# Kernel tuning notes

Measured on AMD Instinct MI355X. Metric: run time of the kernel, lower is better.

Reference implementation:

```python
import jax, jax.numpy as jnp
import numpy as np

MAX_JOINTS = 143

def setup_inputs() -> dict:
    key = jax.random.key(0)
    ks = jax.random.split(key, 8)
    d_model, latent_dim, feat = 256, 512, 13
    s = lambda n: 1.0 / np.sqrt(n)
    return {
        "z": jax.random.normal(ks[0], (32, latent_dim), jnp.float32),
        "W_latent": jax.random.normal(ks[1], (latent_dim, d_model), jnp.float32) * s(latent_dim),
        "b_latent": jnp.zeros((d_model,), jnp.float32),
        "joint_emb": jax.random.normal(ks[2], (MAX_JOINTS, d_model), jnp.float32),
        "frame_emb": jax.random.normal(ks[3], (120, d_model), jnp.float32),
        "ln_gamma": jnp.ones((d_model,), jnp.float32),
        "ln_beta": jnp.zeros((d_model,), jnp.float32),
        "W1": jax.random.normal(ks[4], (d_model, d_model), jnp.float32) * s(d_model),
        "b1": jnp.zeros((d_model,), jnp.float32),
        "W2": jax.random.normal(ks[5], (d_model, feat), jnp.float32) * s(d_model),
        "b2": jnp.zeros((feat,), jnp.float32),
        "max_frames": 120,
    }

def reference(z, W_latent, b_latent, joint_emb, frame_emb, ln_gamma, ln_beta, W1, b1, W2, b2, max_frames):
    # base: [B, d]
    base = z @ W_latent + b_latent
    fe = frame_emb[:max_frames]  # [F, d]
    # three-way broadcast sum -> [B, J, F, d]
    hidden = base[:, None, None, :] + joint_emb[None, :, None, :] + fe[None, None, :, :]
    # LayerNorm over last dim (eps=1e-5, torch default)
    mu = jnp.mean(hidden, axis=-1, keepdims=True)
    var = jnp.mean(jnp.square(hidden - mu), axis=-1, keepdims=True)
    h = (hidden - mu) * jax.lax.rsqrt(var + 1e-5) * ln_gamma + ln_beta
    # MLP: Linear -> exact GELU -> Linear
    h = jax.nn.gelu(h @ W1 + b1, approximate=False)
    out = h @ W2 + b2  # [B, J, F, feat]
    return jnp.transpose(out, (0, 1, 3, 2))  # [B, J, feat, F]
```

## Files before the change

kernel.cpp:

```cpp
#include <hip/hip_runtime.h>
#include <hip/hip_bf16.h>

typedef __bf16 bf16x8 __attribute__((ext_vector_type(8)));
typedef float  f32x4  __attribute__((ext_vector_type(4)));
typedef float  f32x2  __attribute__((ext_vector_type(2)));

#define B_  32
#define J_  143
#define F_  120
#define D_  256
#define L_  512
#define C_  13
#define M_  4576
#define NK  512
#define NNB 384
#define QB  9
#define GRIDC 509
#define CLS 260
#define PXS 388

static __device__ __forceinline__ unsigned short bits(__bf16 h) {
  return __builtin_bit_cast(unsigned short, h);
}

__device__ __forceinline__ f32x2 gelu2(f32x2 u) {
  f32x2 x2 = u * u;
  f32x2 t  = u * (x2 * -0.1029432f + -2.3022082f);
  f32x2 e;
  e.x = __builtin_amdgcn_exp2f(t.x);
  e.y = __builtin_amdgcn_exp2f(t.y);
  f32x2 d = e + 1.0f;
  f32x2 r;
  r.x = __builtin_amdgcn_rcpf(d.x);
  r.y = __builtin_amdgcn_rcpf(d.y);
  return u * r;
}

__global__ __launch_bounds__(256) void prep_kernel(
    const float* __restrict__ z, const float* __restrict__ Wl,
    const float* __restrict__ bl, const float* __restrict__ W1,
    const float* __restrict__ gamma, const float* __restrict__ beta,
    const float* __restrict__ b1, const float* __restrict__ fe,
    const float* __restrict__ W2,
    float* __restrict__ base, unsigned short* __restrict__ BT,
    float* __restrict__ bW1, float* __restrict__ Sfe, float* __restrict__ Sfe2,
    unsigned short* __restrict__ W2T, float* __restrict__ P2f) {
  const int t = threadIdx.x, bid = blockIdx.x;
  const int lane = t & 63, wv = t >> 6;
  __shared__ float zs[L_];
  __shared__ float ra[4], rb[4];
  __shared__ float fegl[256], gl2[256];

  if (bid < 32) {
    zs[t]       = z[bid * L_ + t];
    zs[t + 256] = z[bid * L_ + t + 256];
    __syncthreads();
    float acc = 0.f;
    #pragma unroll 32
    for (int k = 0; k < L_; ++k) acc = __builtin_fmaf(zs[k], Wl[k * D_ + t], acc);
    base[bid * D_ + t] = acc + bl[t];
    return;
  }
  if (bid < 432) {
    const int n = bid - 32;
    if (n < 256) {
      const float w1v = W1[t * D_ + n];
      float a = gamma[t] * w1v;
      float b = beta[t] * w1v;
      const float wg = a;
      #pragma unroll
      for (int m = 1; m < 64; m <<= 1) { a += __shfl_xor(a, m); b += __shfl_xor(b, m); }
      if (lane == 0) { ra[wv] = a; rb[wv] = b; }
      __syncthreads();
      const float cs = ra[0] + ra[1] + ra[2] + ra[3];
      if (t == 0) bW1[n] = rb[0] + rb[1] + rb[2] + rb[3] + b1[n];
      const float m = __builtin_fmaf(cs, -1.f / 256.f, wg);
      const __bf16 hi = (__bf16)m;
      const __bf16 lo = (__bf16)(m - (float)hi);
      BT[n * NK + t]       = bits(hi);
      BT[n * NK + 256 + t] = bits(lo);
    } else if (n < 376) {
      const int f = n - 256;
      const float v = fe[f * D_ + t];
      float a = v, b = v * v;
      #pragma unroll
      for (int m = 1; m < 64; m <<= 1) { a += __shfl_xor(a, m); b += __shfl_xor(b, m); }
      if (lane == 0) { ra[wv] = a; rb[wv] = b; }
      __syncthreads();
      if (t == 0) {
        Sfe[f]  = ra[0] + ra[1] + ra[2] + ra[3];
        Sfe2[f] = rb[0] + rb[1] + rb[2] + rb[3];
      }
      const __bf16 hi = (__bf16)v;
      const __bf16 lo = (__bf16)(v - (float)hi);
      BT[n * NK + t]       = bits(hi);
      BT[n * NK + 256 + t] = bits(lo);
    } else if (n < 384) {
      BT[n * NK + t] = 0; BT[n * NK + 256 + t] = 0;
    } else {
      const int c = n - 384;
      const float v = (c < C_) ? W2[t * C_ + c] : 0.f;
      W2T[c * D_ + t] = bits((__bf16)v);
    }
    return;
  }
  {
    const int f = bid - 432;
    const float fv = fe[f * D_ + t];
    const float gv = gamma[t];
    fegl[t] = fv * gv;
    gl2[t]  = gv;
    float a = fv;
    #pragma unroll
    for (int m = 1; m < 64; m <<= 1) a += __shfl_xor(a, m);
    if (lane == 0) ra[wv] = a;
    __syncthreads();
    const float sfe = ra[0] + ra[1] + ra[2] + ra[3];
    float acc1 = 0.f, acc2 = 0.f;
    #pragma unroll 8
    for (int k = 0; k < 256; ++k) {
      const float w = W1[k * D_ + t];
      acc1 = __builtin_fmaf(fegl[k], w, acc1);
      acc2 = __builtin_fmaf(gl2[k],  w, acc2);
    }
    P2f[f * D_ + t] = __builtin_fmaf(-sfe * (1.f / 256.f), acc2, acc1);
  }
}

__global__ __launch_bounds__(512, 4) void megaC_kernel(
    const float* __restrict__ base, const float* __restrict__ joint,
    const unsigned short* __restrict__ BT, const float* __restrict__ P2f,
    const float* __restrict__ bW1,
    const float* __restrict__ Sfe, const float* __restrict__ Sfe2,
    const unsigned short* __restrict__ W2T, const float* __restrict__ b2,
    float* __restrict__ out) {
  __shared__ float cl[16 * CLS];
  __shared__ float px[16 * PXS];
  __shared__ float bw[256];
  __shared__ float rstdl[QB][128];
  __shared__ float Scl[QB], Sc2l[QB];
  __shared__ __align__(16) unsigned short w2l[4096];

  const int tid  = threadIdx.x;
  const int lane = tid & 63, wv = tid >> 6;
  const int lrow = lane & 15, lgrp = lane >> 4;
  const int bj0  = blockIdx.x * QB;

  #pragma unroll
  for (int i = 0; i < 8; ++i) {
    const int idx = tid + i * 512;
    const int row = idx >> 8, col = idx & 255;
    float v = 0.f;
    if (row < QB) {
      const int bj = min(bj0 + row, M_ - 1);
      const int b = bj / J_, j = bj - b * J_;
      v = base[b * D_ + col] + joint[j * D_ + col];
    }
    cl[row * CLS + col] = v;
  }
  if (tid < 256) {
    bw[tid] = bW1[tid];
    const int rr = tid >> 4;
    const int b0 = tid * 32;
    const int sb = b0 ^ ((rr & 7) << 4);
    *(uint4*)((char*)w2l + sb)        = *(const uint4*)((const char*)W2T + b0);
    *(uint4*)((char*)w2l + (sb ^ 16)) = *(const uint4*)((const char*)W2T + b0 + 16);
  }
  __syncthreads();

  for (int r = wv; r < QB; r += 8) {
    const float4 v4 = *(const float4*)(cl + r * CLS + lane * 4);
    float s = v4.x + v4.y + v4.z + v4.w;
    float q = __builtin_fmaf(v4.x, v4.x,
              __builtin_fmaf(v4.y, v4.y,
              __builtin_fmaf(v4.z, v4.z, v4.w * v4.w)));
    #pragma unroll
    for (int m = 1; m < 64; m <<= 1) { s += __shfl_xor(s, m); q += __shfl_xor(q, m); }
    if (lane == 0) { Scl[r] = s; Sc2l[r] = q; }
  }

  {
    const int colbase = wv * 48;
    f32x4 acc[3] = {};
    #pragma unroll
    for (int s8 = 0; s8 < 8; ++s8) {
      const int k0 = s8 * 32 + lgrp * 8;
      const float4 c0 = *(const float4*)(cl + lrow * CLS + k0);
      const float4 c1 = *(const float4*)(cl + lrow * CLS + k0 + 4);
      const float cc[8] = {c0.x, c0.y, c0.z, c0.w, c1.x, c1.y, c1.z, c1.w};
      bf16x8 ahi, alo;
      #pragma unroll
      for (int e = 0; e < 8; ++e) {
        const __bf16 h = (__bf16)cc[e];
        ahi[e] = h;
        alo[e] = (__bf16)(cc[e] - (float)h);
      }
      bf16x8 bhi[3], blo[3];
      #pragma unroll
      for (int cf = 0; cf < 3; ++cf) {
        const unsigned short* bp =
            BT + (size_t)(colbase + cf * 16 + lrow) * NK + lgrp * 8;
        bhi[cf] = *(const bf16x8*)(bp + s8 * 32);
        blo[cf] = *(const bf16x8*)(bp + 256 + s8 * 32);
      }
      #pragma unroll
      for (int cf = 0; cf < 3; ++cf)
        acc[cf] = __builtin_amdgcn_mfma_f32_16x16x32_bf16(ahi, bhi[cf], acc[cf], 0, 0, 0);
      #pragma unroll
      for (int cf = 0; cf < 3; ++cf)
        acc[cf] = __builtin_amdgcn_mfma_f32_16x16x32_bf16(alo, bhi[cf], acc[cf], 0, 0, 0);
      #pragma unroll
      for (int cf = 0; cf < 3; ++cf)
        acc[cf] = __builtin_amdgcn_mfma_f32_16x16x32_bf16(ahi, blo[cf], acc[cf], 0, 0, 0);
    }
    #pragma unroll
    for (int cf = 0; cf < 3; ++cf)
      #pragma unroll
      for (int r4 = 0; r4 < 4; ++r4)
        px[(lgrp * 4 + r4) * PXS + colbase + cf * 16 + lrow] = acc[cf][r4];
  }
  __syncthreads();

  #pragma unroll
  for (int i = 0; i < 3; ++i) {
    const int idx = tid + i * 512;
    if (idx < QB * 128) {
      const int q = idx >> 7;
      const int fr = idx & 127;
      const int fc = fr < F_ ? fr : F_ - 1;
      const float X = px[q * PXS + 256 + fc];
      const float mu = (Scl[q] + Sfe[fc]) * (1.f / 256.f);
      const float ms = __builtin_fmaf(2.f, X, Sc2l[q] + Sfe2[fc]) * (1.f / 256.f);
      rstdl[q][fr] = rsqrtf(ms - mu * mu + 1e-5f);
    }
  }
  __syncthreads();

  const int r0 = wv * 16 + lrow;
  const int f0 = r0 < F_ ? r0 : F_ - 1;
  float rs[QB];
  #pragma unroll
  for (int q = 0; q < QB; ++q) rs[q] = rstdl[q][r0];
  const float* __restrict__ q0p = P2f + f0 * D_ + lgrp * 8;

  float4 qa0 = *(const float4*)(q0p), qa1 = *(const float4*)(q0p + 4);

  f32x4 acc2[QB] = {};
  #pragma unroll
  for (int s = 0; s < 8; ++s) {
    const int n0 = s * 32 + lgrp * 8;
    float4 na0, na1;
    if (s < 7) {
      na0 = *(const float4*)(q0p + (s + 1) * 32);
      na1 = *(const float4*)(q0p + (s + 1) * 32 + 4);
    }
    const bf16x8 w2f = *(const bf16x8*)((const char*)w2l +
        ((lrow * 512 + n0 * 2) ^ ((lrow & 7) << 4)));
    const float q0v[8] = {qa0.x, qa0.y, qa0.z, qa0.w, qa1.x, qa1.y, qa1.z, qa1.w};
    #pragma unroll
    for (int q = 0; q < QB; ++q) {
      bf16x8 af;
      f32x2 RS; RS.x = rs[q]; RS.y = rs[q];
      #pragma unroll
      for (int ep = 0; ep < 4; ++ep) {
        const int e0 = 2 * ep;
        f32x2 Q0, BV, P;
        Q0.x = q0v[e0]; Q0.y = q0v[e0 + 1];
        BV = *(const f32x2*)(&bw[n0 + e0]);
        P  = *(const f32x2*)(&px[q * PXS + n0 + e0]);
        const f32x2 U = __builtin_elementwise_fma(RS, P + Q0, BV);
        const f32x2 G = gelu2(U);
        af[e0] = (__bf16)G.x; af[e0 + 1] = (__bf16)G.y;
      }
      acc2[q] = __builtin_amdgcn_mfma_f32_16x16x32_bf16(af, w2f, acc2[q], 0, 0, 0);
    }
    qa0 = na0; qa1 = na1;
  }

  if (lrow < C_) {
    const float bias = b2[lrow];
    const int f = wv * 16 + lgrp * 4;
    if (f < F_) {
      #pragma unroll
      for (int q = 0; q < QB; ++q) {
        if (bj0 + q < M_) {
          float4 v;
          v.x = acc2[q][0] + bias;
          v.y = acc2[q][1] + bias;
          v.z = acc2[q][2] + bias;
          v.w = acc2[q][3] + bias;
          *(float4*)(out + (size_t)(bj0 + q) * (C_ * F_) + lrow * F_ + f) = v;
        }
      }
    }
  }
}

extern "C" void kernel_launch(void* const* d_in, const int* in_sizes, int n_in,
                              void* d_out, int out_size, void* d_ws, size_t ws_size,
                              hipStream_t stream) {
  const float* z     = (const float*)d_in[0];
  const float* Wl    = (const float*)d_in[1];
  const float* bl    = (const float*)d_in[2];
  const float* joint = (const float*)d_in[3];
  const float* fe    = (const float*)d_in[4];
  const float* gamma = (const float*)d_in[5];
  const float* beta  = (const float*)d_in[6];
  const float* W1    = (const float*)d_in[7];
  const float* b1    = (const float*)d_in[8];
  const float* W2    = (const float*)d_in[9];
  const float* b2    = (const float*)d_in[10];
  float* out = (float*)d_out;

  char* ws = (char*)d_ws;
  float*          base  = (float*)(ws + 0);
  unsigned short* W2T   = (unsigned short*)(ws + 32768);
  float*          bW1   = (float*)(ws + 40960);
  float*          Sfe   = (float*)(ws + 41984);
  float*          Sfe2  = (float*)(ws + 42496);
  float*          P2f   = (float*)(ws + 65536);
  unsigned short* BT    = (unsigned short*)(ws + 262144);

  prep_kernel<<<552, 256, 0, stream>>>(z, Wl, bl, W1, gamma, beta, b1, fe, W2,
                                       base, BT, bW1, Sfe, Sfe2, W2T, P2f);
  megaC_kernel<<<GRIDC, 512, 0, stream>>>(base, joint, BT, P2f, bW1,
                                          Sfe, Sfe2, W2T, b2, out);
}
```

Before: 76.07 us.

## Shrink per-block batch rows to six and compute rstd inline per thread

Reduces the number of (batch, joint) rows each block handles from nine to six, growing the grid from 509 to 763 blocks and lowering the launch-bounds occupancy hint from 4 to 3. It also drops the shared rstd table and its extra barrier, so each thread now computes its own LayerNorm rstd values directly from px and the per-frame sums. The aim is better load balance across CUs and one fewer sync. In exchange the per-block setup (W2 tile load, first GEMM over 16 padded rows) is amortised over fewer rows, and each thread repeats the rstd arithmetic.

```diff
diff --git a/kernel.cpp b/kernel.cpp
--- a/kernel.cpp
+++ b/kernel.cpp
@@ -13,9 +13,8 @@
 #define C_  13
 #define M_  4576
 #define NK  512
-#define NNB 384
-#define QB  9
-#define GRIDC 509
+#define QB  6
+#define GRIDC 763
 #define CLS 260
 #define PXS 388
 
@@ -127,7 +126,7 @@
   }
 }
 
-__global__ __launch_bounds__(512, 4) void megaC_kernel(
+__global__ __launch_bounds__(512, 3) void megaC_kernel(
     const float* __restrict__ base, const float* __restrict__ joint,
     const unsigned short* __restrict__ BT, const float* __restrict__ P2f,
     const float* __restrict__ bW1,
@@ -135,9 +134,8 @@
     const unsigned short* __restrict__ W2T, const float* __restrict__ b2,
     float* __restrict__ out) {
   __shared__ float cl[16 * CLS];
-  __shared__ float px[16 * PXS];
+  __shared__ float px[QB * PXS];
   __shared__ float bw[256];
-  __shared__ float rstdl[QB][128];
   __shared__ float Scl[QB], Sc2l[QB];
   __shared__ __align__(16) unsigned short w2l[4096];
 
@@ -168,15 +166,15 @@
   }
   __syncthreads();
 
-  for (int r = wv; r < QB; r += 8) {
-    const float4 v4 = *(const float4*)(cl + r * CLS + lane * 4);
+  if (wv < QB) {
+    const float4 v4 = *(const float4*)(cl + wv * CLS + lane * 4);
     float s = v4.x + v4.y + v4.z + v4.w;
     float q = __builtin_fmaf(v4.x, v4.x,
               __builtin_fmaf(v4.y, v4.y,
               __builtin_fmaf(v4.z, v4.z, v4.w * v4.w)));
     #pragma unroll
     for (int m = 1; m < 64; m <<= 1) { s += __shfl_xor(s, m); q += __shfl_xor(q, m); }
-    if (lane == 0) { Scl[r] = s; Sc2l[r] = q; }
+    if (lane == 0) { Scl[wv] = s; Sc2l[wv] = q; }
   }
 
   {
@@ -216,31 +214,26 @@
     #pragma unroll
     for (int cf = 0; cf < 3; ++cf)
       #pragma unroll
-      for (int r4 = 0; r4 < 4; ++r4)
-        px[(lgrp * 4 + r4) * PXS + colbase + cf * 16 + lrow] = acc[cf][r4];
-  }
-  __syncthreads();
-
-  #pragma unroll
-  for (int i = 0; i < 3; ++i) {
-    const int idx = tid + i * 512;
-    if (idx < QB * 128) {
-      const int q = idx >> 7;
-      const int fr = idx & 127;
-      const int fc = fr < F_ ? fr : F_ - 1;
-      const float X = px[q * PXS + 256 + fc];
-      const float mu = (Scl[q] + Sfe[fc]) * (1.f / 256.f);
-      const float ms = __builtin_fmaf(2.f, X, Sc2l[q] + Sfe2[fc]) * (1.f / 256.f);
-      rstdl[q][fr] = rsqrtf(ms - mu * mu + 1e-5f);
-    }
+      for (int r4 = 0; r4 < 4; ++r4) {
+        const int row = lgrp * 4 + r4;
+        if (row < QB)
+          px[row * PXS + colbase + cf * 16 + lrow] = acc[cf][r4];
+      }
   }
   __syncthreads();
 
   const int r0 = wv * 16 + lrow;
   const int f0 = r0 < F_ ? r0 : F_ - 1;
+  const float sfe  = Sfe[f0];
+  const float sfe2 = Sfe2[f0];
   float rs[QB];
   #pragma unroll
-  for (int q = 0; q < QB; ++q) rs[q] = rstdl[q][r0];
+  for (int q = 0; q < QB; ++q) {
+    const float X  = px[q * PXS + 256 + f0];
+    const float mu = (Scl[q] + sfe) * (1.f / 256.f);
+    const float ms = __builtin_fmaf(2.f, X, Sc2l[q] + sfe2) * (1.f / 256.f);
+    rs[q] = rsqrtf(ms - mu * mu + 1e-5f);
+  }
   const float* __restrict__ q0p = P2f + f0 * D_ + lgrp * 8;
 
   float4 qa0 = *(const float4*)(q0p), qa1 = *(const float4*)(q0p + 4);
```

Result: slower. 84.55 us (+11.2%).
